# Kernel tuning notes

Measured on AMD Instinct MI355X. Metric: run time of the kernel, lower is better.

## Reference

```python
import jax, jax.numpy as jnp
import numpy as np

B, N, W = 4, 16384, 4          # batch, npoints, point feature width (xyz + intensity)
M, K = 512, 32                  # nsample keypoints, neighbors per keypoint
DIL = 2.0
NK = int(K * DIL)               # dilated candidate pool
KG = 8                          # knn size inside DGCNN edge-convs
C3 = 256


def _fps(xyz, m):
    """Farthest point sampling. xyz: (B,N,3) -> indices (B,m)."""
    Bb, Nn, _ = xyz.shape
    def step(carry, _):
        mind, cur = carry
        p = jnp.take_along_axis(xyz, cur[:, None, None], axis=1)  # (B,1,3)
        d = jnp.sum((xyz - p) ** 2, axis=-1)                       # (B,N)
        mind = jnp.minimum(mind, d)
        nxt = jnp.argmax(mind, axis=-1).astype(jnp.int32)
        return (mind, nxt), cur
    init = (jnp.full((Bb, Nn), 1e10, xyz.dtype), jnp.zeros((Bb,), jnp.int32))
    _, idx = jax.lax.scan(step, init, None, length=m)
    return jnp.transpose(idx)  # (B,m)


def _edge_conv(x, w, g, b, kg):
    """Dynamic-graph edge conv. x: (G,P,C) -> (G,P,D). Feature = cat(x_j-x_i, x_i)."""
    sq = jnp.sum(x * x, axis=-1)
    d2 = sq[:, :, None] + sq[:, None, :] - 2.0 * jnp.einsum('gpc,gqc->gpq', x, x)
    _, idx = jax.lax.top_k(-d2, kg)                                   # (G,P,kg)
    xj = jnp.take_along_axis(x[:, None], idx[..., None], axis=2)      # (G,P,kg,C)
    ef = jnp.concatenate([xj - x[:, :, None, :],
                          jnp.broadcast_to(x[:, :, None, :], xj.shape)], axis=-1)
    h = jnp.einsum('gpkc,cd->gpkd', ef, w)
    h = jax.nn.relu(g * h + b)  # BN (inference, unit running stats) + ReLU
    return jnp.max(h, axis=2)   # max over graph neighbors


def setup_inputs() -> dict:
    key = jax.random.key(0)
    ks = jax.random.split(key, 12)
    s = 0.05
    inp = {
        'x': jax.random.normal(ks[0], (B, N, W), jnp.float32),
        'rand_idx': jax.random.randint(ks[1], (K,), 0, NK),
        # DGCNN edge-conv params
        'w_e1': jax.random.normal(ks[2], (24, 64), jnp.float32) * s,
        'g1': jnp.ones((64,), jnp.float32), 'b1': jnp.zeros((64,), jnp.float32),
        'w_e2': jax.random.normal(ks[3], (128, C3), jnp.float32) * s,
        'g2': jnp.ones((C3,), jnp.float32), 'b2': jnp.zeros((C3,), jnp.float32),
        # saliency MLP (1x1 conv1d stacks)
        'w_m1': jax.random.normal(ks[4], (C3, C3), jnp.float32) * s,
        'bm1': jnp.zeros((C3,), jnp.float32),
        'gm1': jnp.ones((C3,), jnp.float32), 'bbm1': jnp.zeros((C3,), jnp.float32),
        'w_m2': jax.random.normal(ks[5], (C3, C3), jnp.float32) * s,
        'bm2': jnp.zeros((C3,), jnp.float32),
        'gm2': jnp.ones((C3,), jnp.float32), 'bbm2': jnp.zeros((C3,), jnp.float32),
        'w_m3': jax.random.normal(ks[6], (C3, 1), jnp.float32) * s,
        'bm3': jnp.zeros((1,), jnp.float32),
    }
    return inp


def reference(x, rand_idx, w_e1, g1, b1, w_e2, g2, b2,
              w_m1, bm1, gm1, bbm1, w_m2, bm2, gm2, bbm2, w_m3, bm3):
    rand_idx = rand_idx.astype(jnp.int32)
    # ---- FPS keypoint sampling ----
    node_idx = _fps(x[:, :, :3], M)                                   # (B,M)
    node = jnp.take_along_axis(x, node_idx[:, :, None], axis=1)       # (B,M,W)
    # ---- random dilation encoding: nk-NN then random k of them ----
    nxyz, pxyz = node[:, :, :3], x[:, :, :3]
    d2 = (jnp.sum(nxyz * nxyz, -1)[:, :, None] + jnp.sum(pxyz * pxyz, -1)[:, None, :]
          - 2.0 * jnp.einsum('bmc,bnc->bmn', nxyz, pxyz))             # (B,M,N)
    _, nn = jax.lax.top_k(-d2, NK)                                    # (B,M,NK)
    sel = nn[:, :, rand_idx]                                          # (B,M,K)
    neigh = jnp.take_along_axis(x[:, None], sel[..., None], axis=2)   # (B,M,K,W)
    rel = neigh[..., :3] - nxyz[:, :, None, :]
    dist = jnp.linalg.norm(rel, axis=-1, keepdims=True)
    node_rep = jnp.broadcast_to(node[:, :, None, :], neigh.shape)
    cluster = jnp.concatenate([node_rep, neigh, rel, dist], axis=-1)  # (B,M,K,12)
    random_cluster = jnp.transpose(cluster, (0, 3, 1, 2))             # (B,12,M,K)
    random_xyz = neigh[..., :3]                                       # (B,M,K,3)
    # ---- DGCNN embedding per cluster ----
    g = cluster.reshape(B * M, K, 12)
    h = _edge_conv(g, w_e1, g1, b1, KG)                               # (BM,K,64)
    h = _edge_conv(h, w_e2, g2, b2, KG)                               # (BM,K,256)
    emb = jnp.transpose(h.reshape(B, M, K, C3), (0, 3, 1, 2))         # (B,256,M,K)
    # ---- attention-weighted pooling ----
    x1 = jnp.max(emb, axis=1)                                         # (B,M,K)
    aw = jax.nn.softmax(x1, axis=-1)
    keypoints = jnp.einsum('bmk,bmkc->bcm', aw, random_xyz)           # (B,3,M)
    afm = emb * aw[:, None]                                           # (B,256,M,K)
    gcf = jnp.sum(afm, axis=-1)                                       # (B,256,M)
    # ---- saliency uncertainty MLP ----
    h = jax.nn.relu(gm1[None, :, None] * (jnp.einsum('bcm,cd->bdm', gcf, w_m1)
                                          + bm1[None, :, None]) + bbm1[None, :, None])
    h = jax.nn.relu(gm2[None, :, None] * (jnp.einsum('bcm,cd->bdm', h, w_m2)
                                          + bm2[None, :, None]) + bbm2[None, :, None])
    s = jnp.einsum('bcm,cd->bdm', h, w_m3) + bm3[None, :, None]       # (B,1,M)
    sal = jax.nn.softplus(s)[:, 0, :] + 0.001                         # (B,M)
    return keypoints, sal, random_cluster, afm
```

## Files before the change

kernel.cpp:

```cpp
#include <hip/hip_runtime.h>
#include <cstdint>

#define Bn 4
#define Nn 16384
#define Mn 512
#define Kn 32

#define O_SAL 6144
#define O_RC  8192
#define O_AFM 794624

__device__ __forceinline__ unsigned fkey(float f) {
  unsigned b = __float_as_uint(f);
  return (b & 0x80000000u) ? ~b : (b | 0x80000000u);
}

__device__ __forceinline__ unsigned long long dkey(double d) {
  unsigned long long b = (unsigned long long)__double_as_longlong(d);
  return (b & 0x8000000000000000ull) ? ~b : (b | 0x8000000000000000ull);
}

__global__ __launch_bounds__(256) void sq_kernel(const float* __restrict__ x,
                                                 float* __restrict__ sqp) {
#pragma clang fp contract(off)
  int i = blockIdx.x * 256 + threadIdx.x;
  float4 v = ((const float4*)x)[i];
  float qx = v.x * v.x;
  float qy = v.y * v.y;
  float qz = v.z * v.z;
  sqp[i] = (qx + qy) + qz;
}

__global__ __launch_bounds__(1024) void fps_kernel(const float* __restrict__ x,
                                                   float* __restrict__ node) {
#pragma clang fp contract(off)
  const int b = blockIdx.x;
  const int t = threadIdx.x;
  const float4* xb = (const float4*)(x + (size_t)b * Nn * 4);
  float px[16], py[16], pz[16], mind[16];
  const int base = t * 16;
#pragma unroll
  for (int i = 0; i < 16; ++i) {
    float4 v = xb[base + i];
    px[i] = v.x; py[i] = v.y; pz[i] = v.z;
    mind[i] = 1e10f;
  }
  __shared__ unsigned long long kbuf[2][16];
  float cx, cy, cz;
  {
    float4 v = xb[0];
    cx = v.x; cy = v.y; cz = v.z;
    if (t == 0) ((float4*)node)[b * Mn] = v;
  }
  for (int s = 1; s < Mn; ++s) {
    float bv = -1.0f;
    int bi = 0x7fffffff;
#pragma unroll
    for (int i = 0; i < 16; ++i) {
      float dx = px[i] - cx;
      float dy = py[i] - cy;
      float dz = pz[i] - cz;
      float qx = dx * dx;
      float qy = dy * dy;
      float qz = dz * dz;
      float d = (qx + qy) + qz;
      float mi = fminf(mind[i], d);
      mind[i] = mi;
      if (mi > bv) { bv = mi; bi = base + i; }
    }
    unsigned long long key =
        ((unsigned long long)fkey(bv) << 32) | (unsigned)(~bi);
#pragma unroll
    for (int off = 32; off > 0; off >>= 1) {
      unsigned long long ok = __shfl_down(key, off);
      key = ok > key ? ok : key;
    }
    if ((t & 63) == 0) kbuf[s & 1][t >> 6] = key;
    __syncthreads();
    {
      const unsigned long long* kb = kbuf[s & 1];
      unsigned long long k[16];
#pragma unroll
      for (int w = 0; w < 16; ++w) k[w] = kb[w];
#pragma unroll
      for (int st = 8; st > 0; st >>= 1)
#pragma unroll
        for (int w = 0; w < 8; ++w)
          if (w < st) k[w] = k[w] > k[w + st] ? k[w] : k[w + st];
      int widx = (int)(~(unsigned)(k[0] & 0xFFFFFFFFu));
      float4 nv = xb[widx];
      cx = nv.x; cy = nv.y; cz = nv.z;
      if (t == 0) ((float4*)node)[b * Mn + s] = nv;
    }
  }
}

__global__ __launch_bounds__(256) void knn_kernel(const float* __restrict__ x,
                                                  const float* __restrict__ node,
                                                  const float* __restrict__ sqp,
                                                  const int* __restrict__ rand_idx,
                                                  int* __restrict__ sel) {
#pragma clang fp contract(off)
  const int bm = blockIdx.x;
  const int b = bm >> 9;
  const int t = threadIdx.x;
  const float4* xb = (const float4*)(x + (size_t)b * Nn * 4);
  const float* sq_b = sqp + b * Nn;
  float4 nd = ((const float4*)node)[bm];
  const float nx = nd.x, ny = nd.y, nz = nd.z;
  const float sqmf = (nx * nx + ny * ny) + nz * nz;
  unsigned key[64];
#pragma unroll
  for (int i = 0; i < 64; ++i) {
    int n = t + (i << 8);
    float4 v = xb[n];
    float dot = nx * v.x;
    dot = __builtin_fmaf(ny, v.y, dot);
    dot = __builtin_fmaf(nz, v.z, dot);
    float d2 = (sqmf + sq_b[n]) - 2.0f * dot;
    key[i] = fkey(d2);
  }
  __shared__ unsigned hist[16];
  __shared__ unsigned sh_prefix;
  __shared__ int sh_r;
  unsigned prefix = 0, pmask = 0;
  int r = 95;
  for (int shift = 28; shift >= 0; shift -= 4) {
    if (t < 16) hist[t] = 0;
    __syncthreads();
#pragma unroll
    for (int i = 0; i < 64; ++i) {
      if ((key[i] & pmask) == prefix) atomicAdd(&hist[(key[i] >> shift) & 15], 1u);
    }
    __syncthreads();
    if (t == 0) {
      int rr = r;
      unsigned bin = 0;
      for (unsigned j = 0; j < 16; ++j) {
        int c = (int)hist[j];
        if (rr < c) { bin = j; break; }
        rr -= c;
      }
      sh_prefix = prefix | (bin << shift);
      sh_r = rr;
    }
    __syncthreads();
    prefix = sh_prefix;
    r = sh_r;
    pmask |= (0xFu << shift);
  }
  const unsigned T = prefix;
  __shared__ int cnt;
  __shared__ unsigned long long karr[128];
  if (t == 0) cnt = 0;
  __syncthreads();
#pragma unroll
  for (int i = 0; i < 64; ++i) {
    if (key[i] <= T) {
      int pos = atomicAdd(&cnt, 1);
      if (pos < 128) {
        unsigned n = (unsigned)(t + (i << 8));
        karr[pos] = ((unsigned long long)key[i] << 32) | n;
      }
    }
  }
  __syncthreads();
  const int nc = cnt < 128 ? cnt : 128;
  if (t < 128 && t >= nc) karr[t] = ~0ull;
  for (int k = 2; k <= 128; k <<= 1) {
    for (int j = k >> 1; j > 0; j >>= 1) {
      __syncthreads();
      if (t < 64) {
        int i = ((t & ~(j - 1)) << 1) | (t & (j - 1));
        int ip = i | j;
        unsigned long long ka = karr[i], kb = karr[ip];
        bool asc = ((i & k) == 0);
        if ((ka > kb) == asc) { karr[i] = kb; karr[ip] = ka; }
      }
    }
  }
  __syncthreads();
  if (t < 32) {
    int ri = rand_idx[t];
    sel[bm * 32 + t] = (int)(unsigned)(karr[ri] & 0xFFFFFFFFu);
  }
}

__device__ __forceinline__ void topk8(const unsigned long long* row, unsigned char* nb) {
  unsigned long long bk[8];
  unsigned char bi[8];
#pragma unroll
  for (int k = 0; k < 8; ++k) { bk[k] = ~0ull; bi[k] = 255; }
  for (int q = 0; q < 32; ++q) {
    unsigned long long kv = row[q];
    if (kv < bk[7]) {
      bk[7] = kv; bi[7] = (unsigned char)q;
#pragma unroll
      for (int k = 6; k >= 0; --k) {
        if (bk[k + 1] < bk[k]) {
          unsigned long long tk = bk[k]; bk[k] = bk[k + 1]; bk[k + 1] = tk;
          unsigned char ti = bi[k]; bi[k] = bi[k + 1]; bi[k + 1] = ti;
        }
      }
    }
  }
#pragma unroll
  for (int k = 0; k < 8; ++k) nb[k] = bi[k];
}

__global__ __launch_bounds__(256) void group_kernel(
    const float* __restrict__ x, const float* __restrict__ node,
    const int* __restrict__ sel, const float* __restrict__ w_e1,
    const float* __restrict__ g1, const float* __restrict__ b1,
    const float* __restrict__ w_e2, const float* __restrict__ g2,
    const float* __restrict__ b2, float* __restrict__ out,
    float* __restrict__ gcf) {
#pragma clang fp contract(off)
  const int bm = blockIdx.x;
  const int b = bm >> 9;
  const int m = bm & 511;
  const int t = threadIdx.x;

  __shared__ float cl[32][13];
  __shared__ float h1t[64][36];
  __shared__ float h1p[32][68];
  __shared__ unsigned char nbr[32][8];
  __shared__ double sqs[32];
  __shared__ float part[4][32];
  __shared__ float aws[32];
  __shared__ union U {
    struct {
      unsigned long long keys[32][32];
      float we_a[12][64];
      float we_d[12][64];
      float a1[32][65];
      float cd1[32][65];
    } s;
    float a2[32 * 256];
  } u;

  const float4* xb = (const float4*)(x + (size_t)b * Nn * 4);
  const float4 ndv = ((const float4*)node)[bm];

  if (t < 32) {
    int n = sel[bm * 32 + t];
    float4 v = xb[n];
    float rx = v.x - ndv.x;
    float ry = v.y - ndv.y;
    float rz = v.z - ndv.z;
    float ds = (rx * rx + ry * ry) + rz * rz;
    ds = __fsqrt_rn(ds);
    cl[t][0] = ndv.x; cl[t][1] = ndv.y; cl[t][2] = ndv.z; cl[t][3] = ndv.w;
    cl[t][4] = v.x;   cl[t][5] = v.y;   cl[t][6] = v.z;   cl[t][7] = v.w;
    cl[t][8] = rx;    cl[t][9] = ry;    cl[t][10] = rz;   cl[t][11] = ds;
  }
  for (int i = t; i < 768; i += 256) {
    int row = i >> 6, d = i & 63;
    float wa = w_e1[row * 64 + d];
    float wb = w_e1[(row + 12) * 64 + d];
    u.s.we_a[row][d] = wa;
    u.s.we_d[row][d] = wb - wa;
  }
  __syncthreads();

  for (int i = t; i < 384; i += 256) {
    int c = i >> 5, p = i & 31;
    out[O_RC + (((size_t)(b * 12 + c) * 512) + m) * 32 + p] = cl[p][c];
  }
  if (t < 32) {
    double q[12];
#pragma unroll
    for (int c = 0; c < 12; ++c) {
      double cv = (double)cl[t][c];
      q[c] = cv * cv;
    }
    double s01 = q[0] + q[1];
    double s23 = q[2] + q[3];
    double s45 = q[4] + q[5];
    double s67 = q[6] + q[7];
    double s = (s01 + s23) + (s45 + s67);
    s = s + q[8];
    s = s + q[9];
    s = s + q[10];
    s = s + q[11];
    sqs[t] = s;
  }
  __syncthreads();

  {
    int p = t >> 3, q0 = (t & 7) << 2;
#pragma unroll
    for (int qq = 0; qq < 4; ++qq) {
      int q = q0 + qq;
      double dot = 0.0;
#pragma unroll
      for (int c = 0; c < 12; ++c)
        dot = dot + (double)cl[p][c] * (double)cl[q][c];
      double d2 = (sqs[p] + sqs[q]) - 2.0 * dot;
      u.s.keys[p][q] = dkey(d2);
    }
  }
  __syncthreads();

  if (t < 32) topk8(&u.s.keys[t][0], &nbr[t][0]);
  {
    int d = t & 63, pg = (t >> 6) << 3;
#pragma unroll
    for (int pp = 0; pp < 8; ++pp) {
      int p = pg + pp;
      float aA = 0.f, aD = 0.f;
#pragma unroll
      for (int c = 0; c < 12; ++c) {
        float xv = cl[p][c];
        aA = fmaf(xv, u.s.we_a[c][d], aA);
        aD = fmaf(xv, u.s.we_d[c][d], aD);
      }
      u.s.a1[p][d] = aA;
      u.s.cd1[p][d] = aD;
    }
  }
  __syncthreads();

  {
    int d = t & 63, pg = (t >> 6) << 3;
    float g1v = g1[d], b1v = b1[d];
#pragma unroll
    for (int pp = 0; pp < 8; ++pp) {
      int p = pg + pp;
      float cd = u.s.cd1[p][d];
      float hm = -1e30f;
#pragma unroll
      for (int k = 0; k < 8; ++k) {
        int j = nbr[p][k];
        float hv = fmaf(g1v, u.s.a1[j][d] + cd, b1v);
        hv = fmaxf(hv, 0.f);
        hm = fmaxf(hm, hv);
      }
      h1t[d][p] = hm;
      h1p[p][d] = hm;
    }
  }
  __syncthreads();

  if (t < 32) {
    double r[8];
#pragma unroll
    for (int j = 0; j < 8; ++j) {
      double hv = (double)h1p[t][j];
      r[j] = hv * hv;
    }
#pragma unroll
    for (int blk = 1; blk < 8; ++blk) {
#pragma unroll
      for (int j = 0; j < 8; ++j) {
        double hv = (double)h1p[t][blk * 8 + j];
        r[j] = r[j] + hv * hv;
      }
    }
    double s01 = r[0] + r[1];
    double s23 = r[2] + r[3];
    double s45 = r[4] + r[5];
    double s67 = r[6] + r[7];
    sqs[t] = (s01 + s23) + (s45 + s67);
  }
  __syncthreads();

  {
    int p = t >> 3, q0 = (t & 7) << 2;
#pragma unroll
    for (int qq = 0; qq < 4; ++qq) {
      int q = q0 + qq;
      double dot = 0.0;
      for (int c = 0; c < 64; ++c)
        dot = dot + (double)h1p[p][c] * (double)h1p[q][c];
      double d2 = (sqs[p] + sqs[q]) - 2.0 * dot;
      u.s.keys[p][q] = dkey(d2);
    }
  }
  __syncthreads();

  if (t < 32) topk8(&u.s.keys[t][0], &nbr[t][0]);
  __syncthreads();

  float accD[32];
  float embv[32];
  {
    float accA[32];
#pragma unroll
    for (int p = 0; p < 32; ++p) { accA[p] = 0.f; accD[p] = 0.f; }
    for (int c = 0; c < 64; ++c) {
      float wt = w_e2[c * 256 + t];
      float wb = w_e2[(c + 64) * 256 + t];
      float wd = wb - wt;
      const float4* row = (const float4*)&h1t[c][0];
#pragma unroll
      for (int p4 = 0; p4 < 8; ++p4) {
        float4 hv = row[p4];
        accA[4 * p4 + 0] = fmaf(hv.x, wt, accA[4 * p4 + 0]);
        accA[4 * p4 + 1] = fmaf(hv.y, wt, accA[4 * p4 + 1]);
        accA[4 * p4 + 2] = fmaf(hv.z, wt, accA[4 * p4 + 2]);
        accA[4 * p4 + 3] = fmaf(hv.w, wt, accA[4 * p4 + 3]);
        accD[4 * p4 + 0] = fmaf(hv.x, wd, accD[4 * p4 + 0]);
        accD[4 * p4 + 1] = fmaf(hv.y, wd, accD[4 * p4 + 1]);
        accD[4 * p4 + 2] = fmaf(hv.z, wd, accD[4 * p4 + 2]);
        accD[4 * p4 + 3] = fmaf(hv.w, wd, accD[4 * p4 + 3]);
      }
    }
#pragma unroll
    for (int p = 0; p < 32; ++p) u.a2[p * 256 + t] = accA[p];
  }
  __syncthreads();
  {
    float g2v = g2[t], b2v = b2[t];
#pragma unroll
    for (int p = 0; p < 32; ++p) {
      float cd = accD[p];
      float e = -1e30f;
#pragma unroll
      for (int k = 0; k < 8; ++k) {
        int j = nbr[p][k];
        float hv = fmaf(g2v, u.a2[j * 256 + t] + cd, b2v);
        hv = fmaxf(hv, 0.f);
        e = fmaxf(e, hv);
      }
      embv[p] = e;
    }
  }

#pragma unroll
  for (int p = 0; p < 32; ++p) {
    float v = embv[p];
#pragma unroll
    for (int off = 32; off > 0; off >>= 1) v = fmaxf(v, __shfl_xor(v, off));
    if ((t & 63) == 0) part[t >> 6][p] = v;
  }
  __syncthreads();

  if (t < 32) {
    float x1 = fmaxf(fmaxf(part[0][t], part[1][t]), fmaxf(part[2][t], part[3][t]));
    float mx = x1;
#pragma unroll
    for (int off = 16; off > 0; off >>= 1) mx = fmaxf(mx, __shfl_xor(mx, off));
    float ex = expf(x1 - mx);
    float sm = ex;
#pragma unroll
    for (int off = 16; off > 0; off >>= 1) sm += __shfl_xor(sm, off);
    float aw = ex / sm;
    aws[t] = aw;
#pragma unroll
    for (int c = 0; c < 3; ++c) {
      float kv = aw * cl[t][4 + c];
#pragma unroll
      for (int off = 16; off > 0; off >>= 1) kv += __shfl_xor(kv, off);
      if (t == 0) out[((size_t)(b * 3 + c)) * 512 + m] = kv;
    }
  }
  __syncthreads();

  {
    float gsum = 0.f;
    size_t abase = (size_t)O_AFM + (((size_t)(b * 256 + t)) * 512 + m) * 32;
    float4* ap = (float4*)(out + abase);
#pragma unroll
    for (int p4 = 0; p4 < 8; ++p4) {
      float4 o;
      o.x = embv[4 * p4 + 0] * aws[4 * p4 + 0];
      o.y = embv[4 * p4 + 1] * aws[4 * p4 + 1];
      o.z = embv[4 * p4 + 2] * aws[4 * p4 + 2];
      o.w = embv[4 * p4 + 3] * aws[4 * p4 + 3];
      gsum += o.x; gsum += o.y; gsum += o.z; gsum += o.w;
      ap[p4] = o;
    }
    gcf[((size_t)(b * 256 + t)) * 512 + m] = gsum;
  }
}

__global__ __launch_bounds__(256) void mlp_kernel(
    const float* __restrict__ gcf, const float* __restrict__ w_m1,
    const float* __restrict__ bm1, const float* __restrict__ gm1,
    const float* __restrict__ bbm1, const float* __restrict__ w_m2,
    const float* __restrict__ bm2, const float* __restrict__ gm2,
    const float* __restrict__ bbm2, const float* __restrict__ w_m3,
    const float* __restrict__ bm3, float* __restrict__ out) {
  const int blk = blockIdx.x;
  const int b = blk >> 4;
  const int m0 = (blk & 15) << 5;
  const int t = threadIdx.x;
  __shared__ float sbuf[256 * 36];

#pragma unroll
  for (int i = 0; i < 32; ++i) {
    int c = (t >> 5) + (i << 3);
    int j = t & 31;
    sbuf[c * 36 + j] = gcf[((size_t)(b * 256 + c)) * 512 + m0 + j];
  }
  __syncthreads();

  float acc[32];
#pragma unroll
  for (int j = 0; j < 32; ++j) acc[j] = 0.f;
  for (int c = 0; c < 256; ++c) {
    float wv = w_m1[c * 256 + t];
    const float4* row = (const float4*)&sbuf[c * 36];
#pragma unroll
    for (int j4 = 0; j4 < 8; ++j4) {
      float4 g4 = row[j4];
      acc[4 * j4 + 0] = fmaf(g4.x, wv, acc[4 * j4 + 0]);
      acc[4 * j4 + 1] = fmaf(g4.y, wv, acc[4 * j4 + 1]);
      acc[4 * j4 + 2] = fmaf(g4.z, wv, acc[4 * j4 + 2]);
      acc[4 * j4 + 3] = fmaf(g4.w, wv, acc[4 * j4 + 3]);
    }
  }
  float y[32];
  {
    float gv = gm1[t], bv = bm1[t], bbv = bbm1[t];
#pragma unroll
    for (int j = 0; j < 32; ++j) y[j] = fmaxf(fmaf(gv, acc[j] + bv, bbv), 0.f);
  }
  __syncthreads();
#pragma unroll
  for (int j = 0; j < 32; ++j) sbuf[t * 36 + j] = y[j];
  __syncthreads();

#pragma unroll
  for (int j = 0; j < 32; ++j) acc[j] = 0.f;
  for (int c = 0; c < 256; ++c) {
    float wv = w_m2[c * 256 + t];
    const float4* row = (const float4*)&sbuf[c * 36];
#pragma unroll
    for (int j4 = 0; j4 < 8; ++j4) {
      float4 g4 = row[j4];
      acc[4 * j4 + 0] = fmaf(g4.x, wv, acc[4 * j4 + 0]);
      acc[4 * j4 + 1] = fmaf(g4.y, wv, acc[4 * j4 + 1]);
      acc[4 * j4 + 2] = fmaf(g4.z, wv, acc[4 * j4 + 2]);
      acc[4 * j4 + 3] = fmaf(g4.w, wv, acc[4 * j4 + 3]);
    }
  }
  {
    float gv = gm2[t], bv = bm2[t], bbv = bbm2[t];
#pragma unroll
    for (int j = 0; j < 32; ++j) y[j] = fmaxf(fmaf(gv, acc[j] + bv, bbv), 0.f);
  }
  __syncthreads();
  {
    float w3v = w_m3[t];
#pragma unroll
    for (int j = 0; j < 32; ++j) sbuf[t * 36 + j] = y[j] * w3v;
  }
  __syncthreads();
  if (t < 32) {
    float s = 0.f;
    for (int d = 0; d < 256; ++d) s += sbuf[d * 36 + t];
    s += bm3[0];
    float sal = log1pf(expf(-fabsf(s))) + fmaxf(s, 0.f) + 0.001f;
    out[O_SAL + (size_t)b * 512 + m0 + t] = sal;
  }
}

extern "C" void kernel_launch(void* const* d_in, const int* in_sizes, int n_in,
                              void* d_out, int out_size, void* d_ws, size_t ws_size,
                              hipStream_t stream) {
  (void)in_sizes; (void)n_in; (void)out_size; (void)ws_size;
  const float* x = (const float*)d_in[0];
  const int* rand_idx = (const int*)d_in[1];
  const float* w_e1 = (const float*)d_in[2];
  const float* g1 = (const float*)d_in[3];
  const float* b1 = (const float*)d_in[4];
  const float* w_e2 = (const float*)d_in[5];
  const float* g2 = (const float*)d_in[6];
  const float* b2 = (const float*)d_in[7];
  const float* w_m1 = (const float*)d_in[8];
  const float* bm1 = (const float*)d_in[9];
  const float* gm1 = (const float*)d_in[10];
  const float* bbm1 = (const float*)d_in[11];
  const float* w_m2 = (const float*)d_in[12];
  const float* bm2 = (const float*)d_in[13];
  const float* gm2 = (const float*)d_in[14];
  const float* bbm2 = (const float*)d_in[15];
  const float* w_m3 = (const float*)d_in[16];
  const float* bm3 = (const float*)d_in[17];
  float* out = (float*)d_out;
  char* ws = (char*)d_ws;

  float* node = (float*)ws;
  float* sqp = (float*)(ws + 32768);
  int* sel = (int*)(ws + 32768 + 262144);
  float* gcf = (float*)(ws + 32768 + 262144 + 262144);

  sq_kernel<<<256, 256, 0, stream>>>(x, sqp);
  fps_kernel<<<Bn, 1024, 0, stream>>>(x, node);
  knn_kernel<<<Bn * Mn, 256, 0, stream>>>(x, node, sqp, rand_idx, sel);
  group_kernel<<<Bn * Mn, 256, 0, stream>>>(x, node, sel, w_e1, g1, b1, w_e2,
                                            g2, b2, out, gcf);
  mlp_kernel<<<64, 256, 0, stream>>>(gcf, w_m1, bm1, gm1, bbm1, w_m2, bm2, gm2,
                                     bbm2, w_m3, bm3, out);
}
```

Baseline: 1.795 ms.

## Vectorize FPS distance update with packed FP32 and DPP wave argmax

Rewrites the farthest-point-sampling inner loop to use packed two-wide FP32 subtract, multiply and add through inline assembly, halving the number of distance ALU instructions. The per-thread argmax becomes a max-then-match pass, and the 64-bit shuffle reduction is replaced by a float DPP max reduction followed by a ballot to find the lowest lane holding the maximum. It also pins waves-per-EU. The sequential FPS loop is latency bound, so shortening each iteration's reduction chain is the target. Tie-breaking is meant to keep the smallest index, and the sign-bit key trick assumes distances are non-negative.

```diff
diff --git a/kernel.cpp b/kernel.cpp
--- a/kernel.cpp
+++ b/kernel.cpp
@@ -31,21 +31,50 @@
   sqp[i] = (qx + qy) + qz;
 }
 
-__global__ __launch_bounds__(1024) void fps_kernel(const float* __restrict__ x,
-                                                   float* __restrict__ node) {
+typedef float f2 __attribute__((ext_vector_type(2)));
+__device__ __forceinline__ f2 pk_sub(f2 a, f2 b) {
+  f2 d;
+  asm("v_pk_add_f32 %0, %1, %2 neg_lo:[0,1] neg_hi:[0,1]"
+      : "=v"(d) : "v"(a), "v"(b));
+  return d;
+}
+__device__ __forceinline__ f2 pk_mul(f2 a, f2 b) {
+  f2 d;
+  asm("v_pk_mul_f32 %0, %1, %2" : "=v"(d) : "v"(a), "v"(b));
+  return d;
+}
+__device__ __forceinline__ f2 pk_add(f2 a, f2 b) {
+  f2 d;
+  asm("v_pk_add_f32 %0, %1, %2" : "=v"(d) : "v"(a), "v"(b));
+  return d;
+}
+
+template <int CTRL>
+__device__ __forceinline__ float dppmaxf(float v) {
+  int m = __builtin_amdgcn_update_dpp(__float_as_int(v), __float_as_int(v),
+                                      CTRL, 0xf, 0xf, false);
+  return fmaxf(v, __int_as_float(m));
+}
+
+__global__ __launch_bounds__(1024)
+__attribute__((amdgpu_waves_per_eu(4, 4)))
+void fps_kernel(const float* __restrict__ x, float* __restrict__ node) {
 #pragma clang fp contract(off)
   const int b = blockIdx.x;
   const int t = threadIdx.x;
   const float4* xb = (const float4*)(x + (size_t)b * Nn * 4);
-  float px[16], py[16], pz[16], mind[16];
+  f2 p2x[8], p2y[8], p2z[8], mind2[8];
   const int base = t * 16;
 #pragma unroll
-  for (int i = 0; i < 16; ++i) {
-    float4 v = xb[base + i];
-    px[i] = v.x; py[i] = v.y; pz[i] = v.z;
-    mind[i] = 1e10f;
-  }
-  __shared__ unsigned long long kbuf[2][16];
+  for (int i = 0; i < 8; ++i) {
+    float4 v0 = xb[base + 2 * i];
+    float4 v1 = xb[base + 2 * i + 1];
+    p2x[i] = (f2){v0.x, v1.x};
+    p2y[i] = (f2){v0.y, v1.y};
+    p2z[i] = (f2){v0.z, v1.z};
+    mind2[i] = (f2){1e10f, 1e10f};
+  }
+  __shared__ __align__(16) unsigned long long kbuf[2][16];
   float cx, cy, cz;
   {
     float4 v = xb[0];
@@ -53,29 +82,55 @@
     if (t == 0) ((float4*)node)[b * Mn] = v;
   }
   for (int s = 1; s < Mn; ++s) {
-    float bv = -1.0f;
-    int bi = 0x7fffffff;
-#pragma unroll
-    for (int i = 0; i < 16; ++i) {
-      float dx = px[i] - cx;
-      float dy = py[i] - cy;
-      float dz = pz[i] - cz;
-      float qx = dx * dx;
-      float qy = dy * dy;
-      float qz = dz * dz;
-      float d = (qx + qy) + qz;
-      float mi = fminf(mind[i], d);
-      mind[i] = mi;
-      if (mi > bv) { bv = mi; bi = base + i; }
-    }
-    unsigned long long key =
-        ((unsigned long long)fkey(bv) << 32) | (unsigned)(~bi);
-#pragma unroll
-    for (int off = 32; off > 0; off >>= 1) {
-      unsigned long long ok = __shfl_down(key, off);
-      key = ok > key ? ok : key;
-    }
-    if ((t & 63) == 0) kbuf[s & 1][t >> 6] = key;
+    f2 c2x = (f2){cx, cx}, c2y = (f2){cy, cy}, c2z = (f2){cz, cz};
+#pragma unroll
+    for (int i = 0; i < 8; ++i) {
+      f2 dx = pk_sub(p2x[i], c2x);
+      f2 dy = pk_sub(p2y[i], c2y);
+      f2 dz = pk_sub(p2z[i], c2z);
+      f2 qx = pk_mul(dx, dx);
+      f2 qy = pk_mul(dy, dy);
+      f2 qz = pk_mul(dz, dz);
+      f2 d = pk_add(pk_add(qx, qy), qz);
+      mind2[i].x = fminf(mind2[i].x, d.x);
+      mind2[i].y = fminf(mind2[i].y, d.y);
+    }
+    float a0 = fmaxf(mind2[0].x, mind2[0].y);
+    float a1 = fmaxf(mind2[1].x, mind2[1].y);
+    float a2 = fmaxf(mind2[2].x, mind2[2].y);
+    float a3 = fmaxf(mind2[3].x, mind2[3].y);
+    float a4 = fmaxf(mind2[4].x, mind2[4].y);
+    float a5 = fmaxf(mind2[5].x, mind2[5].y);
+    float a6 = fmaxf(mind2[6].x, mind2[6].y);
+    float a7 = fmaxf(mind2[7].x, mind2[7].y);
+    float b0 = fmaxf(a0, a1);
+    float b1 = fmaxf(a2, a3);
+    float b2 = fmaxf(a4, a5);
+    float b3 = fmaxf(a6, a7);
+    float bv = fmaxf(fmaxf(b0, b1), fmaxf(b2, b3));
+    int isel = 0;
+#pragma unroll
+    for (int i = 15; i >= 0; --i) {
+      float v = (i & 1) ? mind2[i >> 1].y : mind2[i >> 1].x;
+      if (v == bv) isel = i;
+    }
+    float r = bv;
+    r = dppmaxf<0x111>(r);
+    r = dppmaxf<0x112>(r);
+    r = dppmaxf<0x114>(r);
+    r = dppmaxf<0x118>(r);
+    r = dppmaxf<0x142>(r);
+    r = dppmaxf<0x143>(r);
+    float wmax = __int_as_float(__builtin_amdgcn_readlane(__float_as_int(r), 63));
+    unsigned long long ball = __ballot(bv == wmax);
+    int wl = __ffsll(ball) - 1;
+    int widx = __builtin_amdgcn_readlane(base + isel, wl);
+    if ((t & 63) == 0) {
+      unsigned long long key =
+          ((unsigned long long)(__float_as_uint(wmax) | 0x80000000u) << 32) |
+          (unsigned)(~widx);
+      kbuf[s & 1][t >> 6] = key;
+    }
     __syncthreads();
     {
       const unsigned long long* kb = kbuf[s & 1];
@@ -87,8 +142,8 @@
 #pragma unroll
         for (int w = 0; w < 8; ++w)
           if (w < st) k[w] = k[w] > k[w + st] ? k[w] : k[w + st];
-      int widx = (int)(~(unsigned)(k[0] & 0xFFFFFFFFu));
-      float4 nv = xb[widx];
+      int wi = (int)(~(unsigned)(k[0] & 0xFFFFFFFFu));
+      float4 nv = xb[wi];
       cx = nv.x; cy = nv.y; cz = nv.z;
       if (t == 0) ((float4*)node)[b * Mn + s] = nv;
     }
```

Result: no change. 1.762 ms (-1.8%).
